# Kernel optimization log

Hardware: AMD Instinct MI355X
Metric: run time of the kernel (lower is better)

The kernel has to match this reference:

```python
import jax, jax.numpy as jnp
import numpy as np


def setup_inputs() -> dict:
    key = jax.random.key(0)
    k1, k2 = jax.random.split(key)
    B, D = 16384, 256
    return {
        "outputs": jax.random.normal(k1, (B, D), dtype=jnp.float32),
        "targets": jax.random.normal(k2, (B, D), dtype=jnp.float32),
    }


def reference(outputs, targets):
    # Cosine-similarity logits: (o @ t^T) / (||o||_row * ||t||_col)
    logits = outputs @ targets.T                      # [B, B]
    o_norm = jnp.linalg.norm(outputs, axis=1)         # [B]
    t_norm = jnp.linalg.norm(targets, axis=1)         # [B]
    logits = logits / o_norm[:, None] / t_norm[None, :]
    # Cross-entropy with labels = arange(B): mean over rows of (logsumexp - diag logit)
    logZ = jax.nn.logsumexp(logits, axis=1)           # [B]
    diag = jnp.diagonal(logits)                       # [B]
    loss = jnp.mean(logZ - diag)
    return loss
```

## Files before the change

### kernel.cpp

```cpp
#include <hip/hip_runtime.h>
#include <hip/hip_bf16.h>
#include <stdint.h>

#define BROWS 16384
#define DIM   256
#define BM    128
#define NBM   (BROWS / BM)
#define NBNR  16
#define NHALF 16
#define NCHUNK 16

#define LOG2E 1.44269504088896340736f

typedef __attribute__((ext_vector_type(8))) int  i32x8;
typedef __attribute__((ext_vector_type(4))) float f32x4;
typedef unsigned char uchar;

#if __has_builtin(__builtin_amdgcn_exp2f)
#define EXP2(x) __builtin_amdgcn_exp2f(x)
#else
#define EXP2(x) exp2f(x)
#endif

__device__ __forceinline__ void gload_lds16(const void* g, void* l) {
  __builtin_amdgcn_global_load_lds(
      (const __attribute__((address_space(1))) void*)g,
      (__attribute__((address_space(3))) void*)l, 16, 0, 0);
}

__device__ __forceinline__ unsigned q4(float x) {
  float a = fabsf(x);
  unsigned q = (a >= 0.25f) + (a >= 0.75f) + (a >= 1.25f) + (a >= 1.75f) +
               (a >= 2.5f) + (a >= 3.5f) + (a >= 5.0f);
  return q | ((__float_as_uint(x) >> 28) & 8u);
}


__global__ void normalize_both(const float* __restrict__ o,
                               const float* __restrict__ t,
                               uchar* __restrict__ o4,
                               uchar* __restrict__ t4,
                               float* __restrict__ dlog) {
  int row  = blockIdx.x * 4 + (threadIdx.x >> 6);
  int lane = threadIdx.x & 63;
  float4 a = *(reinterpret_cast<const float4*>(o + (size_t)row * DIM) + lane);
  float4 b = *(reinterpret_cast<const float4*>(t + (size_t)row * DIM) + lane);
  float sso = a.x * a.x + a.y * a.y + a.z * a.z + a.w * a.w;
  float sst = b.x * b.x + b.y * b.y + b.z * b.z + b.w * b.w;
  float d   = a.x * b.x + a.y * b.y + a.z * b.z + a.w * b.w;
#pragma unroll
  for (int m = 1; m < 64; m <<= 1) {
    sso += __shfl_xor(sso, m);
    sst += __shfl_xor(sst, m);
    d   += __shfl_xor(d, m);
  }
  float ro = rsqrtf(sso);
  float rt = rsqrtf(sst);
  if (lane == 0) dlog[row] = d * ro * rt;
  float qo = ro * (16.0f * LOG2E);
  float qt = rt * 16.0f;
  unsigned wo = q4(a.x * qo) | (q4(a.y * qo) << 4) |
                (q4(a.z * qo) << 8) | (q4(a.w * qo) << 12);
  unsigned wt = q4(b.x * qt) | (q4(b.y * qt) << 4) |
                (q4(b.z * qt) << 8) | (q4(b.w * qt) << 12);
  size_t taddr = (size_t)(row >> 4) * 2048 + (size_t)((lane >> 3) * 256) +
                 (size_t)((row & 15) * 16) + (size_t)((lane & 7) * 2);
  *reinterpret_cast<unsigned short*>(o4 + taddr) = (unsigned short)wo;
  *reinterpret_cast<unsigned short*>(t4 + taddr) = (unsigned short)wt;
}

__global__ __launch_bounds__(256, 5) void gemm_expsum(
    const uchar* __restrict__ A4,
    const uchar* __restrict__ B4,
    float* __restrict__ partial) {
  __shared__ __align__(16) uchar Bs[2][8192];

  int b   = blockIdx.x;
  int xcd = b & 7;
  int idx = b >> 3;
  int bm  = xcd * 16 + (idx & 15);
  int bnr = idx >> 4;

  int tid  = threadIdx.x;
  int lane = tid & 63;
  int wid  = tid >> 6;

  const uchar* Ap = A4 + (size_t)(bm * 8 + wid * 2) * 2048 + (size_t)lane * 16;
  const uchar* Bg = B4 + (size_t)bnr * 131072;

  i32x8 af[2][2];
#pragma unroll
  for (int m = 0; m < 2; ++m)
#pragma unroll
    for (int kt = 0; kt < 2; ++kt) {
      int4 d = *reinterpret_cast<const int4*>(Ap + m * 2048 + kt * 1024);
      af[m][kt] = (i32x8){d.x, d.y, d.z, d.w, 0, 0, 0, 0};
    }

  float v[8];
#pragma unroll
  for (int j = 0; j < 8; ++j) v[j] = 0.f;

  const f32x4 zero4 = {0.f, 0.f, 0.f, 0.f};

#define STAGE(ht, s)                                                           \
  {                                                                            \
    _Pragma("unroll") for (int p = 0; p < 2; ++p)                              \
        gload_lds16(Bg + (size_t)(ht) * 8192 + p * 4096 + wid * 1024 +         \
                        lane * 16,                                             \
                    (char*)Bs[s] + p * 4096 + wid * 1024);                     \
  }

#define COMPUTE(s)                                                             \
  {                                                                            \
    const uchar* bb = Bs[s];                                                   \
    _Pragma("unroll") for (int n = 0; n < 4; ++n) {                            \
      const uchar* cb = bb + n * 2048 + lane * 16;                             \
      int4 d0 = *reinterpret_cast<const int4*>(cb);                            \
      int4 d1 = *reinterpret_cast<const int4*>(cb + 1024);                     \
      i32x8 b0 = (i32x8){d0.x, d0.y, d0.z, d0.w, 0, 0, 0, 0};                  \
      i32x8 b1 = (i32x8){d1.x, d1.y, d1.z, d1.w, 0, 0, 0, 0};                  \
      _Pragma("unroll") for (int m = 0; m < 2; ++m) {                          \
        f32x4 acc = __builtin_amdgcn_mfma_scale_f32_16x16x128_f8f6f4(          \
            af[m][0], b0, zero4, 4, 4, 0, 0x7B7B7B7B, 0, 0x7B7B7B7B);          \
        acc = __builtin_amdgcn_mfma_scale_f32_16x16x128_f8f6f4(                \
            af[m][1], b1, acc, 4, 4, 0, 0x7B7B7B7B, 0, 0x7B7B7B7B);            \
        v[m * 4 + 0] += EXP2(acc[0]);                                          \
        v[m * 4 + 1] += EXP2(acc[1]);                                          \
        v[m * 4 + 2] += EXP2(acc[2]);                                          \
        v[m * 4 + 3] += EXP2(acc[3]);                                          \
      }                                                                        \
    }                                                                          \
  }

  STAGE(0, 0);
  __syncthreads();
#pragma unroll
  for (int ht = 0; ht < NHALF; ++ht) {
    if (ht < NHALF - 1) STAGE(ht + 1, (ht + 1) & 1);
    COMPUTE(ht & 1);
    if (ht < NHALF - 1) __syncthreads();
  }
#undef STAGE
#undef COMPUTE

#pragma unroll
  for (int s = 0; s < 3; ++s) {
    const int len = 8 >> s;
    const int bit = (lane >> s) & 1;
#pragma unroll
    for (int t = 0; t < 4; ++t) {
      if (t < (len >> 1)) {
        float a = v[2 * t], b2 = v[2 * t + 1];
        float recv = __shfl_xor(bit ? a : b2, 1 << s);
        v[t] = (bit ? b2 : a) + recv;
      }
    }
  }
  v[0] += __shfl_xor(v[0], 8);
  if ((lane & 8) == 0) {
    int j   = lane & 7;
    int sub = lane >> 4;
    int row = bm * BM + wid * 32 + (j >> 2) * 16 + sub * 4 + (j & 3);
    partial[(size_t)row * NCHUNK + bnr] = v[0];
  }
}

__global__ void row_finish(const float* __restrict__ partial,
                           const float* __restrict__ dlog,
                           float* __restrict__ rowloss) {
  int row = blockIdx.x * 256 + threadIdx.x;
  const float4* p = reinterpret_cast<const float4*>(partial + (size_t)row * NCHUNK);
  float4 p0 = p[0], p1 = p[1], p2 = p[2], p3 = p[3];
  float s = (p0.x + p0.y + p0.z + p0.w) + (p1.x + p1.y + p1.z + p1.w) +
            (p2.x + p2.y + p2.z + p2.w) + (p3.x + p3.y + p3.z + p3.w);
  rowloss[row] = logf(s) - dlog[row];
}

__global__ void final_reduce(const float* __restrict__ rl, float* __restrict__ out) {
  __shared__ float sm[16];
  float s = 0.f;
  for (int i = threadIdx.x; i < BROWS; i += 1024) s += rl[i];
#pragma unroll
  for (int m = 1; m < 64; m <<= 1) s += __shfl_xor(s, m);
  int wid = threadIdx.x >> 6, lane = threadIdx.x & 63;
  if (lane == 0) sm[wid] = s;
  __syncthreads();
  if (wid == 0) {
    float v = (lane < 16) ? sm[lane] : 0.f;
#pragma unroll
    for (int m = 1; m < 16; m <<= 1) v += __shfl_xor(v, m);
    if (lane == 0) out[0] = v / (float)BROWS;
  }
}

extern "C" void kernel_launch(void* const* d_in, const int* in_sizes, int n_in,
                              void* d_out, int out_size, void* d_ws, size_t ws_size,
                              hipStream_t stream) {
  const float* outputs = (const float*)d_in[0];
  const float* targets = (const float*)d_in[1];
  float* out = (float*)d_out;
  char* ws = (char*)d_ws;

  uchar* o4      = (uchar*)ws;
  uchar* t4      = (uchar*)(ws + (size_t)2 * 1024 * 1024);
  float* partial = (float*)(ws + (size_t)4 * 1024 * 1024);
  float* dlog    = (float*)(ws + (size_t)6 * 1024 * 1024);
  float* rowloss = (float*)(ws + (size_t)6 * 1024 * 1024 + 65536);

  normalize_both<<<BROWS / 4, 256, 0, stream>>>(outputs, targets, o4, t4, dlog);
  gemm_expsum<<<NBM * NBNR, 256, 0, stream>>>(o4, t4, partial);
  row_finish<<<BROWS / 256, 256, 0, stream>>>(partial, dlog, rowloss);
  final_reduce<<<1, 1024, 0, stream>>>(rowloss, out);
}
```

Measured before the change: 62.74 us.

## Split GEMM block column tiles across two wave groups with 512 threads

The GEMM+exp-sum block goes from 256 to 512 threads. Two wave groups share the same A rows, and each group handles half of the B column tiles in a staged chunk. Each thread now issues one LDS-direct load per stage instead of two. Partial sums per row double to 32 chunks, so row_finish reads twice as many values. The change aims to raise the number of waves resident per CU and hide MFMA/exp latency, at the cost of more register pressure under the new launch bounds and more partial-sum traffic.

Result: no change. 62.64 us (-0.2%).

```diff
diff --git a/kernel.cpp b/kernel.cpp
--- a/kernel.cpp
+++ b/kernel.cpp
@@ -8,7 +8,7 @@
 #define NBM   (BROWS / BM)
 #define NBNR  16
 #define NHALF 16
-#define NCHUNK 16
+#define NCHUNK 32
 
 #define LOG2E 1.44269504088896340736f
 
@@ -69,7 +69,7 @@
   *reinterpret_cast<unsigned short*>(t4 + taddr) = (unsigned short)wt;
 }
 
-__global__ __launch_bounds__(256, 5) void gemm_expsum(
+__global__ __launch_bounds__(512, 8) void gemm_expsum(
     const uchar* __restrict__ A4,
     const uchar* __restrict__ B4,
     float* __restrict__ partial) {
@@ -84,8 +84,10 @@
   int tid  = threadIdx.x;
   int lane = tid & 63;
   int wid  = tid >> 6;
-
-  const uchar* Ap = A4 + (size_t)(bm * 8 + wid * 2) * 2048 + (size_t)lane * 16;
+  int wr   = wid & 3;
+  int wch  = wid >> 2;
+
+  const uchar* Ap = A4 + (size_t)(bm * 8 + wr * 2) * 2048 + (size_t)lane * 16;
   const uchar* Bg = B4 + (size_t)bnr * 131072;
 
   i32x8 af[2][2];
@@ -102,34 +104,33 @@
   for (int j = 0; j < 8; ++j) v[j] = 0.f;
 
   const f32x4 zero4 = {0.f, 0.f, 0.f, 0.f};
+  i32x8 bop = (i32x8){0, 0, 0, 0, 0, 0, 0, 0};
 
 #define STAGE(ht, s)                                                           \
-  {                                                                            \
-    _Pragma("unroll") for (int p = 0; p < 2; ++p)                              \
-        gload_lds16(Bg + (size_t)(ht) * 8192 + p * 4096 + wid * 1024 +         \
-                        lane * 16,                                             \
-                    (char*)Bs[s] + p * 4096 + wid * 1024);                     \
-  }
+  gload_lds16(Bg + (size_t)(ht) * 8192 + wid * 1024 + lane * 16,               \
+              (char*)Bs[s] + wid * 1024 + lane * 16);
 
 #define COMPUTE(s)                                                             \
   {                                                                            \
     const uchar* bb = Bs[s];                                                   \
-    _Pragma("unroll") for (int n = 0; n < 4; ++n) {                            \
-      const uchar* cb = bb + n * 2048 + lane * 16;                             \
+    _Pragma("unroll") for (int nn = 0; nn < 2; ++nn) {                         \
+      const uchar* cb = bb + (wch * 2 + nn) * 2048 + lane * 16;                \
       int4 d0 = *reinterpret_cast<const int4*>(cb);                            \
+      bop[0] = d0.x; bop[1] = d0.y; bop[2] = d0.z; bop[3] = d0.w;              \
+      f32x4 a0 = __builtin_amdgcn_mfma_scale_f32_16x16x128_f8f6f4(             \
+          af[0][0], bop, zero4, 4, 4, 0, 0x7B7B7B7B, 0, 0x7B7B7B7B);           \
+      f32x4 a1 = __builtin_amdgcn_mfma_scale_f32_16x16x128_f8f6f4(             \
+          af[1][0], bop, zero4, 4, 4, 0, 0x7B7B7B7B, 0, 0x7B7B7B7B);           \
       int4 d1 = *reinterpret_cast<const int4*>(cb + 1024);                     \
-      i32x8 b0 = (i32x8){d0.x, d0.y, d0.z, d0.w, 0, 0, 0, 0};                  \
-      i32x8 b1 = (i32x8){d1.x, d1.y, d1.z, d1.w, 0, 0, 0, 0};                  \
-      _Pragma("unroll") for (int m = 0; m < 2; ++m) {                          \
-        f32x4 acc = __builtin_amdgcn_mfma_scale_f32_16x16x128_f8f6f4(          \
-            af[m][0], b0, zero4, 4, 4, 0, 0x7B7B7B7B, 0, 0x7B7B7B7B);          \
-        acc = __builtin_amdgcn_mfma_scale_f32_16x16x128_f8f6f4(                \
-            af[m][1], b1, acc, 4, 4, 0, 0x7B7B7B7B, 0, 0x7B7B7B7B);            \
-        v[m * 4 + 0] += EXP2(acc[0]);                                          \
-        v[m * 4 + 1] += EXP2(acc[1]);                                          \
-        v[m * 4 + 2] += EXP2(acc[2]);                                          \
-        v[m * 4 + 3] += EXP2(acc[3]);                                          \
-      }                                                                        \
+      bop[0] = d1.x; bop[1] = d1.y; bop[2] = d1.z; bop[3] = d1.w;              \
+      a0 = __builtin_amdgcn_mfma_scale_f32_16x16x128_f8f6f4(                   \
+          af[0][1], bop, a0, 4, 4, 0, 0x7B7B7B7B, 0, 0x7B7B7B7B);              \
+      a1 = __builtin_amdgcn_mfma_scale_f32_16x16x128_f8f6f4(                   \
+          af[1][1], bop, a1, 4, 4, 0, 0x7B7B7B7B, 0, 0x7B7B7B7B);              \
+      v[0] += EXP2(a0[0]); v[1] += EXP2(a0[1]);                                \
+      v[2] += EXP2(a0[2]); v[3] += EXP2(a0[3]);                                \
+      v[4] += EXP2(a1[0]); v[5] += EXP2(a1[1]);                                \
+      v[6] += EXP2(a1[2]); v[7] += EXP2(a1[3]);                                \
     }                                                                          \
   }
 
@@ -161,8 +162,8 @@
   if ((lane & 8) == 0) {
     int j   = lane & 7;
     int sub = lane >> 4;
-    int row = bm * BM + wid * 32 + (j >> 2) * 16 + sub * 4 + (j & 3);
-    partial[(size_t)row * NCHUNK + bnr] = v[0];
+    int row = bm * BM + wr * 32 + (j >> 2) * 16 + sub * 4 + (j & 3);
+    partial[(size_t)row * NCHUNK + ((bnr << 1) | wch)] = v[0];
   }
 }
 
@@ -171,9 +172,12 @@
                            float* __restrict__ rowloss) {
   int row = blockIdx.x * 256 + threadIdx.x;
   const float4* p = reinterpret_cast<const float4*>(partial + (size_t)row * NCHUNK);
-  float4 p0 = p[0], p1 = p[1], p2 = p[2], p3 = p[3];
-  float s = (p0.x + p0.y + p0.z + p0.w) + (p1.x + p1.y + p1.z + p1.w) +
-            (p2.x + p2.y + p2.z + p2.w) + (p3.x + p3.y + p3.z + p3.w);
+  float s = 0.f;
+#pragma unroll
+  for (int q = 0; q < 8; ++q) {
+    float4 pq = p[q];
+    s += (pq.x + pq.y) + (pq.z + pq.w);
+  }
   rowloss[row] = logf(s) - dlog[row];
 }
 
@@ -209,7 +213,7 @@
   float* rowloss = (float*)(ws + (size_t)6 * 1024 * 1024 + 65536);
 
   normalize_both<<<BROWS / 4, 256, 0, stream>>>(outputs, targets, o4, t4, dlog);
-  gemm_expsum<<<NBM * NBNR, 256, 0, stream>>>(o4, t4, partial);
+  gemm_expsum<<<NBM * NBNR, 512, 0, stream>>>(o4, t4, partial);
   row_finish<<<BROWS / 256, 256, 0, stream>>>(partial, dlog, rowloss);
   final_reduce<<<1, 1024, 0, stream>>>(rowloss, out);
 }
```
